# Kernel optimization log

Measured on AMD Instinct MI355X. Metric: run time of the kernel, lower is better.

The kernel has to match this reference:

```python
import jax, jax.numpy as jnp
import numpy as np

B, N = 8, 64
EMB, CD, NL = 32, 24, 3          # emb_dim, cloud_dim, output degrees l=0,1,2 (cloudord)
NB, H = 3, 100                   # radial basis count, radial hidden width
RADIUS = 2.0                     # neighborradius
CLOUD_OUT = CD * NL**2 + EMB     # 24*9 + 32 = 248 (cloud_res concat)
RES_OUT = 2 * CLOUD_OUT          # 496 (AtomResiduals doubles channels)
FF = 128                         # ffl1size // 1


def spherical_harmonics(u):
    # real SH on unit vectors, se3cnn component order (y,z,x for l=1)
    x, y, z = u[..., 0], u[..., 1], u[..., 2]
    Y0 = jnp.full(x.shape + (1,), 0.28209479177, dtype=u.dtype)
    c1 = 0.48860251190
    Y1 = c1 * jnp.stack([y, z, x], -1)
    c2a, c2b = 1.09254843059, 0.31539156525
    Y2 = jnp.stack([c2a * x * y, c2a * y * z, c2b * (3.0 * z * z - 1.0),
                    c2a * x * z, 0.5 * c2a * (x * x - y * y)], -1)
    return [Y0, Y1, Y2]


def setup_inputs() -> dict:
    key = jax.random.key(0)
    ks = jax.random.split(key, 12)
    g = lambda i, shape, s=0.1: jax.random.normal(ks[i], shape, jnp.float32) * s
    return dict(
        xyz=jax.random.normal(ks[0], (B, N, 3), jnp.float32),
        features=jax.random.randint(ks[1], (B, N), 0, 6),
        emb=g(2, (6, EMB), 1.0),
        rW1=g(3, (NB, H)), rb1=jnp.zeros((H,), jnp.float32),
        rW2=g(4, (H, H)), rb2=jnp.zeros((H,), jnp.float32),
        rW3=g(5, (H, NL * CD * EMB)), rb3=jnp.zeros((NL * CD * EMB,), jnp.float32),
        resW=g(6, (CLOUD_OUT, CLOUD_OUT)), resb=jnp.zeros((CLOUD_OUT,), jnp.float32),
        res_gamma=jnp.ones((CLOUD_OUT,), jnp.float32),
        res_beta=jnp.zeros((CLOUD_OUT,), jnp.float32),
        cW=g(7, (RES_OUT, FF)), cb=jnp.zeros((FF,), jnp.float32),
        c_gamma=jnp.ones((FF,), jnp.float32), c_beta=jnp.zeros((FF,), jnp.float32),
        oW=g(8, (FF, 1)), ob=jnp.zeros((1,), jnp.float32),
    )


def reference(xyz, features, emb, rW1, rb1, rW2, rb2, rW3, rb3,
              resW, resb, res_gamma, res_beta, cW, cb, c_gamma, c_beta, oW, ob):
    eps = 1e-8
    f = emb[features]                                     # [B,N,EMB] scalar (l=0) features
    rij = xyz[:, None, :, :] - xyz[:, :, None, :]         # r_j - r_i  [B,N,N,3]
    d = jnp.sqrt(jnp.sum(rij * rij, -1) + eps)            # [B,N,N]
    mask = ((d < RADIUS) & (~jnp.eye(N, dtype=bool))).astype(f.dtype)
    # CosineBasisModel: cos^2 bumps centered at linspace(0, RADIUS, NB)
    radii = jnp.linspace(0.0, RADIUS, NB)
    step = radii[1] - radii[0]
    u = jnp.abs(d[..., None] - radii) / step
    basis = jnp.where(u < 1.0, jnp.cos(0.5 * jnp.pi * u) ** 2, 0.0)  # [B,N,N,NB]
    sp = lambda x: jax.nn.softplus(5.0 * x) / 5.0          # rescaled Softplus(beta=5)
    h = sp(basis @ rW1 + rb1)
    h = sp(h @ rW2 + rb2)
    R = (h @ rW3 + rb3).reshape(B, N, N, NL, CD, EMB)      # per-pair radial weights
    # contract scalar input channels first (keeps intermediates small): [B,N,N,L,U]
    t = jnp.einsum('bijluv,bjv->bijlu', R, f) / jnp.sqrt(float(EMB))
    Ys = spherical_harmonics(rij / d[..., None])
    inv = (1.0 / jnp.sqrt(jnp.maximum(mask.sum(-1), 1.0)))[:, :, None, None]
    outs = []
    for l, Y in enumerate(Ys):
        o = jnp.einsum('bij,bijm,biju->bium', mask, Y, t[..., l, :])  # [B,N,U,2l+1]
        outs.append((o * inv).reshape(B, N, CD * (2 * l + 1)))
    conv = jnp.concatenate(outs, -1)                       # [B,N,216]
    feats = jnp.concatenate([f, conv], -1)                 # cloud_res concat [B,N,248]
    # AtomResiduals: Linear -> BatchNorm(batch stats) -> relu, concat with input
    x2 = feats.reshape(B * N, CLOUD_OUT) @ resW + resb
    mu, var = x2.mean(0), x2.var(0)
    x2 = jax.nn.relu((x2 - mu) / jnp.sqrt(var + 1e-5) * res_gamma + res_beta)
    feats = jnp.concatenate([feats, x2.reshape(B, N, CLOUD_OUT)], -1)  # [B,N,496]
    pooled = feats.mean(1)                                 # mean collation [B,496]
    h2 = jax.nn.leaky_relu(pooled @ cW + cb, 0.01)
    mu2, var2 = h2.mean(0), h2.var(0)
    h2 = jax.nn.leaky_relu((h2 - mu2) / jnp.sqrt(var2 + 1e-5) * c_gamma + c_beta, 0.01)
    return jax.nn.sigmoid(h2 @ oW + ob)                    # [B,1]
```

## Files before the change

### kernel.cpp

```cpp
#include <hip/hip_runtime.h>
#include <hip/hip_bf16.h>

#define BB   8
#define NN   64
#define EMB  32
#define CD   24
#define HH   100
#define LU   72
#define COUT 248
#define RESO 496
#define FF   128

__device__ __forceinline__ float sp5(float x) {
    float z = 5.0f * x;
    float t = __expf(-fabsf(z));
    return 0.2f * (fmaxf(z, 0.0f) + __logf(1.0f + t));
}
__device__ __forceinline__ float4 ld4(const float* p) { return *reinterpret_cast<const float4*>(p); }
__device__ __forceinline__ void st4(float* p, float4 v) { *reinterpret_cast<float4*>(p) = v; }
__device__ __forceinline__ void fma4(float4& a, float s, float4 w) {
    a.x = fmaf(s, w.x, a.x); a.y = fmaf(s, w.y, a.y);
    a.z = fmaf(s, w.z, a.z); a.w = fmaf(s, w.w, a.w);
}

__global__ __launch_bounds__(256) void k0_w3f(
    const float* __restrict__ rW3, const float* __restrict__ rb3,
    const float* __restrict__ emb, float* __restrict__ W3f_all, float* __restrict__ tb_all)
{
    const int t = blockIdx.x / 10, kc = blockIdx.x % 10;
    __shared__ float embt[EMB];
    if (threadIdx.x < EMB) embt[threadIdx.x] = emb[t * EMB + threadIdx.x];
    __syncthreads();
    for (int idx = threadIdx.x; idx < 10 * LU; idx += 256) {
        const int k = kc * 10 + idx / LU, lu = idx % LU;
        const float* w = rW3 + (size_t)k * (LU * EMB) + lu * EMB;
        float acc = 0.f;
#pragma unroll
        for (int v4 = 0; v4 < EMB / 4; ++v4) {
            float4 wv = ld4(w + 4 * v4);
            acc += wv.x * embt[4 * v4] + wv.y * embt[4 * v4 + 1]
                 + wv.z * embt[4 * v4 + 2] + wv.w * embt[4 * v4 + 3];
        }
        W3f_all[(size_t)t * HH * LU + k * LU + lu] = acc;
    }
    if (kc == 0 && threadIdx.x < LU) {
        const float* w = rb3 + threadIdx.x * EMB;
        float acc = 0.f;
        for (int v = 0; v < EMB; ++v) acc += w[v] * embt[v];
        tb_all[t * LU + threadIdx.x] = acc;
    }
}

__global__ __launch_bounds__(256) void k1_pairs(
    const float* __restrict__ xyz, const int* __restrict__ feat,
    const float* __restrict__ rW1, const float* __restrict__ rb1,
    const float* __restrict__ rW2, const float* __restrict__ rb2,
    const float* __restrict__ W3f_all, const float* __restrict__ tb_all,
    float* __restrict__ tbuf)
{
    const int b = blockIdx.x >> 6, j = blockIdx.x & 63;
    const int tid = threadIdx.x;

    __shared__ __align__(16) float rW2s[HH * HH];
    __shared__ __align__(16) float W3fs[HH * LU];
    __shared__ __align__(16) float h1T[HH * NN];
    __shared__ __align__(16) float h2T[HH * NN];
    __shared__ __align__(16) float rW1s[3 * HH];
    __shared__ __align__(16) float rb1s[HH];
    __shared__ __align__(16) float rb2s[HH];
    __shared__ __align__(16) float tbs[LU];
    __shared__ __align__(16) float xi[NN * 3];

    const int type = feat[b * NN + j];
    for (int idx = tid; idx < HH * HH / 4; idx += 256) st4(&rW2s[idx * 4], ld4(&rW2[idx * 4]));
    {
        const float* src = W3f_all + (size_t)type * HH * LU;
        for (int idx = tid; idx < HH * LU / 4; idx += 256) st4(&W3fs[idx * 4], ld4(&src[idx * 4]));
    }
    if (tid < 75)                 st4(&rW1s[tid * 4], ld4(&rW1[tid * 4]));
    if (tid >= 80 && tid < 105)   st4(&rb1s[(tid - 80) * 4], ld4(&rb1[(tid - 80) * 4]));
    if (tid >= 112 && tid < 137)  st4(&rb2s[(tid - 112) * 4], ld4(&rb2[(tid - 112) * 4]));
    if (tid >= 144 && tid < 162)  st4(&tbs[(tid - 144) * 4], ld4(&tb_all[type * LU + (tid - 144) * 4]));
    if (tid >= 168 && tid < 216)  st4(&xi[(tid - 168) * 4], ld4(&xyz[b * NN * 3 + (tid - 168) * 4]));
    __syncthreads();

    {
        const int ik = tid & 63, ug = tid >> 6;
        const float dx = xi[j * 3 + 0] - xi[ik * 3 + 0];
        const float dy = xi[j * 3 + 1] - xi[ik * 3 + 1];
        const float dz = xi[j * 3 + 2] - xi[ik * 3 + 2];
        const float d = sqrtf(dx * dx + dy * dy + dz * dz + 1e-8f);
        float bas[3];
#pragma unroll
        for (int r = 0; r < 3; ++r) {
            float u = fabsf(d - (float)r);
            float c = cosf(1.57079632679489662f * u);
            bas[r] = (u < 1.0f) ? c * c : 0.0f;
        }
#pragma unroll
        for (int uu = 0; uu < 25; ++uu) {
            const int u = ug * 25 + uu;
            float v = rb1s[u] + bas[0] * rW1s[u] + bas[1] * rW1s[HH + u] + bas[2] * rW1s[2 * HH + u];
            h1T[u * NN + ik] = sp5(v);
        }
    }
    __syncthreads();

    if (tid < 200) {
        const int ut = tid % 25, ig = tid / 25;
        float4 a[8];
        {
            float4 b0 = ld4(&rb2s[4 * ut]);
#pragma unroll
            for (int m = 0; m < 8; ++m) a[m] = b0;
        }
        for (int k = 0; k < HH; ++k) {
            float4 w  = ld4(&rW2s[k * HH + 4 * ut]);
            float4 hA = ld4(&h1T[k * NN + 8 * ig]);
            float4 hB = ld4(&h1T[k * NN + 8 * ig + 4]);
            fma4(a[0], hA.x, w); fma4(a[1], hA.y, w); fma4(a[2], hA.z, w); fma4(a[3], hA.w, w);
            fma4(a[4], hB.x, w); fma4(a[5], hB.y, w); fma4(a[6], hB.z, w); fma4(a[7], hB.w, w);
        }
#pragma unroll
        for (int m = 0; m < 8; ++m) {
            a[m].x = sp5(a[m].x); a[m].y = sp5(a[m].y); a[m].z = sp5(a[m].z); a[m].w = sp5(a[m].w);
        }
        st4(&h2T[(4 * ut + 0) * NN + 8 * ig],     make_float4(a[0].x, a[1].x, a[2].x, a[3].x));
        st4(&h2T[(4 * ut + 0) * NN + 8 * ig + 4], make_float4(a[4].x, a[5].x, a[6].x, a[7].x));
        st4(&h2T[(4 * ut + 1) * NN + 8 * ig],     make_float4(a[0].y, a[1].y, a[2].y, a[3].y));
        st4(&h2T[(4 * ut + 1) * NN + 8 * ig + 4], make_float4(a[4].y, a[5].y, a[6].y, a[7].y));
        st4(&h2T[(4 * ut + 2) * NN + 8 * ig],     make_float4(a[0].z, a[1].z, a[2].z, a[3].z));
        st4(&h2T[(4 * ut + 2) * NN + 8 * ig + 4], make_float4(a[4].z, a[5].z, a[6].z, a[7].z));
        st4(&h2T[(4 * ut + 3) * NN + 8 * ig],     make_float4(a[0].w, a[1].w, a[2].w, a[3].w));
        st4(&h2T[(4 * ut + 3) * NN + 8 * ig + 4], make_float4(a[4].w, a[5].w, a[6].w, a[7].w));
    }
    __syncthreads();

    if (tid < 144) {
        const int lut = tid % 18, ig = tid / 18;
        float4 a[8];
        {
            float4 t0 = ld4(&tbs[4 * lut]);
#pragma unroll
            for (int m = 0; m < 8; ++m) a[m] = t0;
        }
        for (int k = 0; k < HH; ++k) {
            float4 w  = ld4(&W3fs[k * LU + 4 * lut]);
            float4 hA = ld4(&h2T[k * NN + 8 * ig]);
            float4 hB = ld4(&h2T[k * NN + 8 * ig + 4]);
            fma4(a[0], hA.x, w); fma4(a[1], hA.y, w); fma4(a[2], hA.z, w); fma4(a[3], hA.w, w);
            fma4(a[4], hB.x, w); fma4(a[5], hB.y, w); fma4(a[6], hB.z, w); fma4(a[7], hB.w, w);
        }
        const float s = 0.17677669529663688f;
#pragma unroll
        for (int m = 0; m < 8; ++m) {
            const int i = 8 * ig + m;
            float* dst = (float*)&tbuf[((size_t)(b * NN + i) * NN + j) * LU + 4 * lut];
            st4(dst, make_float4(a[m].x * s, a[m].y * s, a[m].z * s, a[m].w * s));
        }
    }
}

__global__ __launch_bounds__(256) void k2_conv(
    const float* __restrict__ xyz, const int* __restrict__ feat,
    const float* __restrict__ emb, const float* __restrict__ tbuf,
    const float* __restrict__ resW, const float* __restrict__ resb,
    float* __restrict__ feats, float* __restrict__ x2pre)
{
    const int b = blockIdx.x >> 6, i = blockIdx.x & 63;
    const int tid = threadIdx.x;
    __shared__ __align__(16) float xj[NN * 3];
    __shared__ __align__(16) float mYT[9 * 68];
    __shared__ __align__(16) float tlT[LU * 68];
    __shared__ __align__(16) float fs[COUT];
    __shared__ float inv_s;

    if (tid < 48) st4(&xj[tid * 4], ld4(&xyz[b * NN * 3 + tid * 4]));
    if (tid >= 64 && tid < 96) fs[tid - 64] = emb[feat[b * NN + i] * EMB + (tid - 64)];
    {
        const float* src = tbuf + (size_t)blockIdx.x * (NN * LU);
        for (int idx = tid; idx < NN * LU; idx += 256) {
            const int jj = idx / LU, lu = idx - jj * LU;
            tlT[lu * 68 + jj] = src[idx];
        }
    }
    __syncthreads();
    if (tid < 64) {
        const int jj = tid;
        float dx = xj[jj * 3 + 0] - xj[i * 3 + 0];
        float dy = xj[jj * 3 + 1] - xj[i * 3 + 1];
        float dz = xj[jj * 3 + 2] - xj[i * 3 + 2];
        float d = sqrtf(dx * dx + dy * dy + dz * dz + 1e-8f);
        float m = (d < 2.0f && jj != i) ? 1.0f : 0.0f;
        float ux = dx / d, uy = dy / d, uz = dz / d;
        mYT[0 * 68 + jj] = m * 0.28209479177f;
        mYT[1 * 68 + jj] = m * 0.48860251190f * uy;
        mYT[2 * 68 + jj] = m * 0.48860251190f * uz;
        mYT[3 * 68 + jj] = m * 0.48860251190f * ux;
        mYT[4 * 68 + jj] = m * 1.09254843059f * ux * uy;
        mYT[5 * 68 + jj] = m * 1.09254843059f * uy * uz;
        mYT[6 * 68 + jj] = m * 0.31539156525f * (3.0f * uz * uz - 1.0f);
        mYT[7 * 68 + jj] = m * 1.09254843059f * ux * uz;
        mYT[8 * 68 + jj] = m * 0.54627421529f * (ux * ux - uy * uy);
        unsigned long long bal = __ballot(m > 0.5f);
        if (jj == 0) inv_s = rsqrtf(fmaxf((float)__popcll(bal), 1.0f));
    }
    __syncthreads();

    if (tid < 216) {
        int l, u, m, yoff;
        if (tid < 24)      { l = 0; u = tid; m = 0; yoff = 0; }
        else if (tid < 96) { int q = tid - 24; l = 1; u = q / 3; m = q % 3; yoff = 1; }
        else               { int q = tid - 96; l = 2; u = q / 5; m = q % 5; yoff = 4; }
        const int lu = l * CD + u, yr = yoff + m;
        float acc = 0.f;
#pragma unroll
        for (int j4 = 0; j4 < 16; ++j4) {
            float4 y = ld4(&mYT[yr * 68 + 4 * j4]);
            float4 t = ld4(&tlT[lu * 68 + 4 * j4]);
            acc += y.x * t.x + y.y * t.y + y.z * t.z + y.w * t.w;
        }
        fs[EMB + tid] = acc * inv_s;
    }
    __syncthreads();

    const size_t row = (size_t)blockIdx.x;
    for (int c = tid; c < COUT; c += 256) feats[row * COUT + c] = fs[c];
    if (tid < COUT) {
        float acc = resb[tid];
        for (int k = 0; k < COUT; ++k) acc = fmaf(fs[k], resW[k * COUT + tid], acc);
        x2pre[row * COUT + tid] = acc;
    }
}

__global__ __launch_bounds__(256) void k4_stats(
    const float* __restrict__ x2pre, float* __restrict__ stats)
{
    const int c = blockIdx.x, tid = threadIdx.x;
    float s = 0.f, s2 = 0.f;
    for (int r = tid; r < BB * NN; r += 256) {
        const float v = x2pre[(size_t)r * COUT + c];
        s += v; s2 += v * v;
    }
    __shared__ float rs[256], rq[256];
    rs[tid] = s; rq[tid] = s2;
    __syncthreads();
    for (int off = 128; off > 0; off >>= 1) {
        if (tid < off) { rs[tid] += rs[tid + off]; rq[tid] += rq[tid + off]; }
        __syncthreads();
    }
    if (tid == 0) {
        const float mu = rs[0] * (1.0f / 512.0f);
        const float var = rq[0] * (1.0f / 512.0f) - mu * mu;
        stats[c] = mu;
        stats[COUT + c] = 1.0f / sqrtf(var + 1e-5f);
    }
}

__global__ __launch_bounds__(512) void k5_pool(
    const float* __restrict__ feats, const float* __restrict__ x2pre,
    const float* __restrict__ stats,
    const float* __restrict__ gamma, const float* __restrict__ beta,
    float* __restrict__ pooledT)
{
    const int b = blockIdx.x, c = threadIdx.x;
    if (c >= RESO) return;
    float acc = 0.f;
    if (c < COUT) {
        for (int i = 0; i < NN; ++i) acc += feats[(size_t)(b * NN + i) * COUT + c];
    } else {
        const int cc = c - COUT;
        const float mu = stats[cc], rstd = stats[COUT + cc];
        const float g = gamma[cc], be = beta[cc];
        for (int i = 0; i < NN; ++i) {
            const float v = (x2pre[(size_t)(b * NN + i) * COUT + cc] - mu) * rstd * g + be;
            acc += fmaxf(v, 0.f);
        }
    }
    pooledT[c * BB + b] = acc * (1.0f / (float)NN);
}

__global__ __launch_bounds__(128) void k6_head(
    const float* __restrict__ pooledT,
    const float* __restrict__ cW, const float* __restrict__ cb,
    const float* __restrict__ c_gamma, const float* __restrict__ c_beta,
    const float* __restrict__ oW, const float* __restrict__ ob,
    float* __restrict__ out)
{
    const int o = threadIdx.x;
    __shared__ __align__(16) float psT[RESO * BB];
    __shared__ __align__(16) float red[FF * BB];
    for (int idx = o; idx < RESO * BB / 4; idx += 128) st4(&psT[idx * 4], ld4(&pooledT[idx * 4]));
    __syncthreads();
    float4 aA = make_float4(0.f, 0.f, 0.f, 0.f), aB = aA;
    for (int k = 0; k < RESO; ++k) {
        float w = cW[k * FF + o];
        float4 pA = ld4(&psT[k * BB]);
        float4 pB = ld4(&psT[k * BB + 4]);
        fma4(aA, w, pA); fma4(aB, w, pB);
    }
    const float cbv = cb[o];
    float h[8] = { aA.x + cbv, aA.y + cbv, aA.z + cbv, aA.w + cbv,
                   aB.x + cbv, aB.y + cbv, aB.z + cbv, aB.w + cbv };
    float mu = 0.f;
#pragma unroll
    for (int q = 0; q < 8; ++q) { h[q] = (h[q] >= 0.f) ? h[q] : 0.01f * h[q]; mu += h[q]; }
    mu *= 0.125f;
    float var = 0.f;
#pragma unroll
    for (int q = 0; q < 8; ++q) { float dd = h[q] - mu; var += dd * dd; }
    var *= 0.125f;
    const float rstd = 1.0f / sqrtf(var + 1e-5f);
    const float g = c_gamma[o], be = c_beta[o], wo = oW[o];
#pragma unroll
    for (int q = 0; q < 8; ++q) {
        float v = (h[q] - mu) * rstd * g + be;
        h[q] = ((v >= 0.f) ? v : 0.01f * v) * wo;
    }
    st4(&red[o * 8],     make_float4(h[0], h[1], h[2], h[3]));
    st4(&red[o * 8 + 4], make_float4(h[4], h[5], h[6], h[7]));
    __syncthreads();
    for (int off = 64; off >= 1; off >>= 1) {
        if (o < off) {
            float4 x0 = ld4(&red[o * 8]),     y0 = ld4(&red[(o + off) * 8]);
            float4 x1 = ld4(&red[o * 8 + 4]), y1 = ld4(&red[(o + off) * 8 + 4]);
            st4(&red[o * 8],     make_float4(x0.x + y0.x, x0.y + y0.y, x0.z + y0.z, x0.w + y0.w));
            st4(&red[o * 8 + 4], make_float4(x1.x + y1.x, x1.y + y1.y, x1.z + y1.z, x1.w + y1.w));
        }
        __syncthreads();
    }
    if (o < BB) out[o] = 1.0f / (1.0f + __expf(-(red[o] + ob[0])));
}

extern "C" void kernel_launch(void* const* d_in, const int* in_sizes, int n_in,
                              void* d_out, int out_size, void* d_ws, size_t ws_size,
                              hipStream_t stream)
{
    const float* xyz  = (const float*)d_in[0];
    const int*   feat = (const int*)  d_in[1];
    const float* emb  = (const float*)d_in[2];
    const float* rW1  = (const float*)d_in[3];
    const float* rb1  = (const float*)d_in[4];
    const float* rW2  = (const float*)d_in[5];
    const float* rb2  = (const float*)d_in[6];
    const float* rW3  = (const float*)d_in[7];
    const float* rb3  = (const float*)d_in[8];
    const float* resW = (const float*)d_in[9];
    const float* resb = (const float*)d_in[10];
    const float* res_gamma = (const float*)d_in[11];
    const float* res_beta  = (const float*)d_in[12];
    const float* cW   = (const float*)d_in[13];
    const float* cb   = (const float*)d_in[14];
    const float* c_gamma = (const float*)d_in[15];
    const float* c_beta  = (const float*)d_in[16];
    const float* oW   = (const float*)d_in[17];
    const float* ob   = (const float*)d_in[18];
    float* out = (float*)d_out;

    char* ws = (char*)d_ws;
    float* tbuf    = (float*)ws;
    float* W3f_all = (float*)(ws + 9437184);
    float* tb_all  = (float*)(ws + 9437184 + 172800);
    float* feats   = (float*)(ws + 9437184 + 172800 + 1728);
    float* x2pre   = feats + 512 * COUT;
    float* stats   = x2pre + 512 * COUT;
    float* pooledT = stats + 2 * COUT;

    k0_w3f  <<<60, 256, 0, stream>>>(rW3, rb3, emb, W3f_all, tb_all);
    k1_pairs<<<BB * NN, 256, 0, stream>>>(xyz, feat, rW1, rb1, rW2, rb2, W3f_all, tb_all, tbuf);
    k2_conv <<<BB * NN, 256, 0, stream>>>(xyz, feat, emb, tbuf, resW, resb, feats, x2pre);
    k4_stats<<<COUT, 256, 0, stream>>>(x2pre, stats);
    k5_pool <<<BB, 512, 0, stream>>>(feats, x2pre, stats, res_gamma, res_beta, pooledT);
    k6_head <<<1, 128, 0, stream>>>(pooledT, cW, cb, c_gamma, c_beta, oW, ob, out);
}
```

Measured before the change: 191.9 us.

## Fuse BN stats into conv via atomics, read weights from global, relayout tbuf

Drops the separate column-statistics kernel and the feats buffer: the conv kernel now atomically accumulates column sums, sums of squares and pooled features, and the first kernel zeros those accumulators. The pair kernel stops staging rW2, rW1 and the biases in shared memory and reads them from global/cache instead. This cuts LDS use per block, which may raise occupancy. The tbuf layout is flipped so the pair kernel writes contiguously, and the conv kernel now does strided gathers. Atomics add contention and non-deterministic summation order, and the one-pass variance formula is less numerically stable.

New measurement: 203.8 us. 6.2% more time.

```diff
diff --git a/kernel.cpp b/kernel.cpp
--- a/kernel.cpp
+++ b/kernel.cpp
@@ -25,8 +25,12 @@
 
 __global__ __launch_bounds__(256) void k0_w3f(
     const float* __restrict__ rW3, const float* __restrict__ rb3,
-    const float* __restrict__ emb, float* __restrict__ W3f_all, float* __restrict__ tb_all)
-{
+    const float* __restrict__ emb, float* __restrict__ W3f_all, float* __restrict__ tb_all,
+    float* __restrict__ accz)
+{
+    if (blockIdx.x == 0) {
+        for (int idx = threadIdx.x; idx < 2 * COUT + BB * COUT; idx += 256) accz[idx] = 0.f;
+    }
     const int t = blockIdx.x / 10, kc = blockIdx.x % 10;
     __shared__ float embt[EMB];
     if (threadIdx.x < EMB) embt[threadIdx.x] = emb[t * EMB + threadIdx.x];
@@ -56,32 +60,22 @@
     const float* __restrict__ rW1, const float* __restrict__ rb1,
     const float* __restrict__ rW2, const float* __restrict__ rb2,
     const float* __restrict__ W3f_all, const float* __restrict__ tb_all,
-    float* __restrict__ tbuf)
+    float* __restrict__ tbufJ)
 {
     const int b = blockIdx.x >> 6, j = blockIdx.x & 63;
     const int tid = threadIdx.x;
 
-    __shared__ __align__(16) float rW2s[HH * HH];
     __shared__ __align__(16) float W3fs[HH * LU];
     __shared__ __align__(16) float h1T[HH * NN];
     __shared__ __align__(16) float h2T[HH * NN];
-    __shared__ __align__(16) float rW1s[3 * HH];
-    __shared__ __align__(16) float rb1s[HH];
-    __shared__ __align__(16) float rb2s[HH];
-    __shared__ __align__(16) float tbs[LU];
     __shared__ __align__(16) float xi[NN * 3];
 
     const int type = feat[b * NN + j];
-    for (int idx = tid; idx < HH * HH / 4; idx += 256) st4(&rW2s[idx * 4], ld4(&rW2[idx * 4]));
     {
         const float* src = W3f_all + (size_t)type * HH * LU;
         for (int idx = tid; idx < HH * LU / 4; idx += 256) st4(&W3fs[idx * 4], ld4(&src[idx * 4]));
     }
-    if (tid < 75)                 st4(&rW1s[tid * 4], ld4(&rW1[tid * 4]));
-    if (tid >= 80 && tid < 105)   st4(&rb1s[(tid - 80) * 4], ld4(&rb1[(tid - 80) * 4]));
-    if (tid >= 112 && tid < 137)  st4(&rb2s[(tid - 112) * 4], ld4(&rb2[(tid - 112) * 4]));
-    if (tid >= 144 && tid < 162)  st4(&tbs[(tid - 144) * 4], ld4(&tb_all[type * LU + (tid - 144) * 4]));
-    if (tid >= 168 && tid < 216)  st4(&xi[(tid - 168) * 4], ld4(&xyz[b * NN * 3 + (tid - 168) * 4]));
+    if (tid < 48) st4(&xi[tid * 4], ld4(&xyz[b * NN * 3 + tid * 4]));
     __syncthreads();
 
     {
@@ -97,10 +91,10 @@
             float c = cosf(1.57079632679489662f * u);
             bas[r] = (u < 1.0f) ? c * c : 0.0f;
         }
-#pragma unroll
+#pragma unroll 5
         for (int uu = 0; uu < 25; ++uu) {
             const int u = ug * 25 + uu;
-            float v = rb1s[u] + bas[0] * rW1s[u] + bas[1] * rW1s[HH + u] + bas[2] * rW1s[2 * HH + u];
+            float v = rb1[u] + bas[0] * rW1[u] + bas[1] * rW1[HH + u] + bas[2] * rW1[2 * HH + u];
             h1T[u * NN + ik] = sp5(v);
         }
     }
@@ -110,12 +104,13 @@
         const int ut = tid % 25, ig = tid / 25;
         float4 a[8];
         {
-            float4 b0 = ld4(&rb2s[4 * ut]);
+            float4 b0 = ld4(&rb2[4 * ut]);
 #pragma unroll
             for (int m = 0; m < 8; ++m) a[m] = b0;
         }
+#pragma unroll 4
         for (int k = 0; k < HH; ++k) {
-            float4 w  = ld4(&rW2s[k * HH + 4 * ut]);
+            float4 w  = ld4(&rW2[k * HH + 4 * ut]);
             float4 hA = ld4(&h1T[k * NN + 8 * ig]);
             float4 hB = ld4(&h1T[k * NN + 8 * ig + 4]);
             fma4(a[0], hA.x, w); fma4(a[1], hA.y, w); fma4(a[2], hA.z, w); fma4(a[3], hA.w, w);
@@ -140,10 +135,11 @@
         const int lut = tid % 18, ig = tid / 18;
         float4 a[8];
         {
-            float4 t0 = ld4(&tbs[4 * lut]);
+            float4 t0 = ld4(&tb_all[type * LU + 4 * lut]);
 #pragma unroll
             for (int m = 0; m < 8; ++m) a[m] = t0;
         }
+#pragma unroll 4
         for (int k = 0; k < HH; ++k) {
             float4 w  = ld4(&W3fs[k * LU + 4 * lut]);
             float4 hA = ld4(&h2T[k * NN + 8 * ig]);
@@ -152,20 +148,21 @@
             fma4(a[4], hB.x, w); fma4(a[5], hB.y, w); fma4(a[6], hB.z, w); fma4(a[7], hB.w, w);
         }
         const float s = 0.17677669529663688f;
+        float* base = &tbufJ[((size_t)(b * NN + j)) * (NN * LU)];
 #pragma unroll
         for (int m = 0; m < 8; ++m) {
             const int i = 8 * ig + m;
-            float* dst = (float*)&tbuf[((size_t)(b * NN + i) * NN + j) * LU + 4 * lut];
-            st4(dst, make_float4(a[m].x * s, a[m].y * s, a[m].z * s, a[m].w * s));
+            st4(&base[i * LU + 4 * lut], make_float4(a[m].x * s, a[m].y * s, a[m].z * s, a[m].w * s));
         }
     }
 }
 
 __global__ __launch_bounds__(256) void k2_conv(
     const float* __restrict__ xyz, const int* __restrict__ feat,
-    const float* __restrict__ emb, const float* __restrict__ tbuf,
+    const float* __restrict__ emb, const float* __restrict__ tbufJ,
     const float* __restrict__ resW, const float* __restrict__ resb,
-    float* __restrict__ feats, float* __restrict__ x2pre)
+    float* __restrict__ x2pre, float* __restrict__ colsum,
+    float* __restrict__ colsq, float* __restrict__ pooledF)
 {
     const int b = blockIdx.x >> 6, i = blockIdx.x & 63;
     const int tid = threadIdx.x;
@@ -178,10 +175,9 @@
     if (tid < 48) st4(&xj[tid * 4], ld4(&xyz[b * NN * 3 + tid * 4]));
     if (tid >= 64 && tid < 96) fs[tid - 64] = emb[feat[b * NN + i] * EMB + (tid - 64)];
     {
-        const float* src = tbuf + (size_t)blockIdx.x * (NN * LU);
         for (int idx = tid; idx < NN * LU; idx += 256) {
             const int jj = idx / LU, lu = idx - jj * LU;
-            tlT[lu * 68 + jj] = src[idx];
+            tlT[lu * 68 + jj] = tbufJ[((size_t)(b * NN + jj)) * (NN * LU) + i * LU + lu];
         }
     }
     __syncthreads();
@@ -224,60 +220,35 @@
     }
     __syncthreads();
 
-    const size_t row = (size_t)blockIdx.x;
-    for (int c = tid; c < COUT; c += 256) feats[row * COUT + c] = fs[c];
     if (tid < COUT) {
         float acc = resb[tid];
         for (int k = 0; k < COUT; ++k) acc = fmaf(fs[k], resW[k * COUT + tid], acc);
-        x2pre[row * COUT + tid] = acc;
-    }
-}
-
-__global__ __launch_bounds__(256) void k4_stats(
-    const float* __restrict__ x2pre, float* __restrict__ stats)
-{
-    const int c = blockIdx.x, tid = threadIdx.x;
-    float s = 0.f, s2 = 0.f;
-    for (int r = tid; r < BB * NN; r += 256) {
-        const float v = x2pre[(size_t)r * COUT + c];
-        s += v; s2 += v * v;
-    }
-    __shared__ float rs[256], rq[256];
-    rs[tid] = s; rq[tid] = s2;
-    __syncthreads();
-    for (int off = 128; off > 0; off >>= 1) {
-        if (tid < off) { rs[tid] += rs[tid + off]; rq[tid] += rq[tid + off]; }
-        __syncthreads();
-    }
-    if (tid == 0) {
-        const float mu = rs[0] * (1.0f / 512.0f);
-        const float var = rq[0] * (1.0f / 512.0f) - mu * mu;
-        stats[c] = mu;
-        stats[COUT + c] = 1.0f / sqrtf(var + 1e-5f);
-    }
-}
-
-__global__ __launch_bounds__(512) void k5_pool(
-    const float* __restrict__ feats, const float* __restrict__ x2pre,
-    const float* __restrict__ stats,
+        x2pre[(size_t)blockIdx.x * COUT + tid] = acc;
+        atomicAdd(&colsum[tid], acc);
+        atomicAdd(&colsq[tid], acc * acc);
+        atomicAdd(&pooledF[b * COUT + tid], fs[tid]);
+    }
+}
+
+__global__ __launch_bounds__(256) void k5_pool(
+    const float* __restrict__ x2pre, const float* __restrict__ colsum,
+    const float* __restrict__ colsq, const float* __restrict__ pooledF,
     const float* __restrict__ gamma, const float* __restrict__ beta,
     float* __restrict__ pooledT)
 {
     const int b = blockIdx.x, c = threadIdx.x;
-    if (c >= RESO) return;
+    if (c >= COUT) return;
+    pooledT[c * BB + b] = pooledF[b * COUT + c] * (1.0f / (float)NN);
+    const float mu   = colsum[c] * (1.0f / 512.0f);
+    const float var  = colsq[c] * (1.0f / 512.0f) - mu * mu;
+    const float rstd = 1.0f / sqrtf(var + 1e-5f);
+    const float g = gamma[c], be = beta[c];
     float acc = 0.f;
-    if (c < COUT) {
-        for (int i = 0; i < NN; ++i) acc += feats[(size_t)(b * NN + i) * COUT + c];
-    } else {
-        const int cc = c - COUT;
-        const float mu = stats[cc], rstd = stats[COUT + cc];
-        const float g = gamma[cc], be = beta[cc];
-        for (int i = 0; i < NN; ++i) {
-            const float v = (x2pre[(size_t)(b * NN + i) * COUT + cc] - mu) * rstd * g + be;
-            acc += fmaxf(v, 0.f);
-        }
-    }
-    pooledT[c * BB + b] = acc * (1.0f / (float)NN);
+    for (int i = 0; i < NN; ++i) {
+        const float v = (x2pre[(size_t)(b * NN + i) * COUT + c] - mu) * rstd * g + be;
+        acc += fmaxf(v, 0.f);
+    }
+    pooledT[(COUT + c) * BB + b] = acc * (1.0f / (float)NN);
 }
 
 __global__ __launch_bounds__(128) void k6_head(
@@ -293,6 +264,7 @@
     for (int idx = o; idx < RESO * BB / 4; idx += 128) st4(&psT[idx * 4], ld4(&pooledT[idx * 4]));
     __syncthreads();
     float4 aA = make_float4(0.f, 0.f, 0.f, 0.f), aB = aA;
+#pragma unroll 4
     for (int k = 0; k < RESO; ++k) {
         float w = cW[k * FF + o];
         float4 pA = ld4(&psT[k * BB]);
@@ -358,18 +330,19 @@
     float* out = (float*)d_out;
 
     char* ws = (char*)d_ws;
-    float* tbuf    = (float*)ws;
+    float* tbufJ   = (float*)ws;
     float* W3f_all = (float*)(ws + 9437184);
     float* tb_all  = (float*)(ws + 9437184 + 172800);
-    float* feats   = (float*)(ws + 9437184 + 172800 + 1728);
-    float* x2pre   = feats + 512 * COUT;
-    float* stats   = x2pre + 512 * COUT;
-    float* pooledT = stats + 2 * COUT;
-
-    k0_w3f  <<<60, 256, 0, stream>>>(rW3, rb3, emb, W3f_all, tb_all);
-    k1_pairs<<<BB * NN, 256, 0, stream>>>(xyz, feat, rW1, rb1, rW2, rb2, W3f_all, tb_all, tbuf);
-    k2_conv <<<BB * NN, 256, 0, stream>>>(xyz, feat, emb, tbuf, resW, resb, feats, x2pre);
-    k4_stats<<<COUT, 256, 0, stream>>>(x2pre, stats);
-    k5_pool <<<BB, 512, 0, stream>>>(feats, x2pre, stats, res_gamma, res_beta, pooledT);
+    float* x2pre   = (float*)(ws + 9437184 + 172800 + 1728);
+    float* colsum  = x2pre + 512 * COUT;
+    float* colsq   = colsum + COUT;
+    float* pooledF = colsq + COUT;
+    float* pooledT = pooledF + BB * COUT;
+
+    k0_w3f  <<<60, 256, 0, stream>>>(rW3, rb3, emb, W3f_all, tb_all, colsum);
+    k1_pairs<<<BB * NN, 256, 0, stream>>>(xyz, feat, rW1, rb1, rW2, rb2, W3f_all, tb_all, tbufJ);
+    k2_conv <<<BB * NN, 256, 0, stream>>>(xyz, feat, emb, tbufJ, resW, resb,
+                                          x2pre, colsum, colsq, pooledF);
+    k5_pool <<<BB, 256, 0, stream>>>(x2pre, colsum, colsq, pooledF, res_gamma, res_beta, pooledT);
     k6_head <<<1, 128, 0, stream>>>(pooledT, cW, cb, c_gamma, c_beta, oW, ob, out);
 }
```
